# Kernel tuning notes

Hardware: AMD Instinct MI355X
Metric: run time of the kernel (lower is better)

Reference implementation:

```python
import jax, jax.numpy as jnp
import numpy as np


def setup_inputs() -> dict:
    key = jax.random.key(0)
    ks = jax.random.split(key, 7)
    SEQ, B, IN, H, OUT = 1024, 1024, 57, 128, 18
    return {
        "line_tensor": jax.random.normal(ks[0], (SEQ, B, IN), dtype=jnp.float32),
        "W_ih": jax.random.normal(ks[1], (H, IN), dtype=jnp.float32) * 0.1,
        "b_ih": jax.random.normal(ks[2], (H,), dtype=jnp.float32) * 0.1,
        "W_hh": jax.random.normal(ks[3], (H, H), dtype=jnp.float32) * 0.1,
        "b_hh": jax.random.normal(ks[4], (H,), dtype=jnp.float32) * 0.1,
        "W_ho": jax.random.normal(ks[5], (OUT, H), dtype=jnp.float32) * 0.1,
        "b_ho": jax.random.normal(ks[6], (OUT,), dtype=jnp.float32) * 0.1,
    }


def reference(line_tensor, W_ih, b_ih, W_hh, b_hh, W_ho, b_ho):
    # Elman RNN: h_t = tanh(i2h(x_t) + h2h(h_{t-1})); output = log_softmax(h2o(h_T))
    B = line_tensor.shape[1]
    H = W_hh.shape[0]
    h0 = jnp.zeros((B, H), dtype=line_tensor.dtype)

    def step(h, x):  # x: [B, IN], h: [B, H]
        h = jnp.tanh(x @ W_ih.T + b_ih + h @ W_hh.T + b_hh)
        return h, None

    hT, _ = jax.lax.scan(step, h0, line_tensor)
    logits = hT @ W_ho.T + b_ho  # [B, OUT]
    out = jax.nn.log_softmax(logits, axis=1)
    return (out, hT)
```

## Files before the change

### kernel.cpp

```cpp
#include <hip/hip_runtime.h>
#include <math.h>

#define SEQ   1024
#define BATCH 1024
#define IN_F  57
#define H_F   128
#define OUT_F 18
#define MROWS 16
#define HSTR  136
#define XSTR  72
#define NT    512

typedef __attribute__((ext_vector_type(8))) short bf8;
typedef __attribute__((ext_vector_type(4))) float f32x4;

static __device__ __forceinline__ short f2bf(float f) {
    unsigned u = __builtin_bit_cast(unsigned, f);
    u = (u + 0x7FFFu + ((u >> 16) & 1u)) >> 16;
    return (short)u;
}
static __device__ __forceinline__ float bf2f(short s) {
    unsigned u = ((unsigned)(unsigned short)s) << 16;
    return __builtin_bit_cast(float, u);
}

__global__ __launch_bounds__(NT) void rnn_mfma_kernel(
    const float* __restrict__ X,
    const float* __restrict__ W_ih,
    const float* __restrict__ b_ih,
    const float* __restrict__ W_hh,
    const float* __restrict__ b_hh,
    const float* __restrict__ W_ho,
    const float* __restrict__ b_ho,
    float* __restrict__ out)
{
    const int tid  = threadIdx.x;
    const int lane = tid & 63;
    const int wv   = tid >> 6;
    const int n16  = lane & 15;
    const int quad = lane >> 4;
    const int b0   = blockIdx.x * MROWS;

    __shared__ short h_lds[2][MROWS][HSTR];
    __shared__ short x_lds[2][MROWS][XSTR];
    __shared__ float logits_lds[MROWS][OUT_F];
    __shared__ float red_lds[MROWS][2];

    const int j0 = wv * 16 + n16;

    const float* wp0 = W_hh + j0 * H_F + quad * 8;
#define LDW8(P) ({ \
        f32x4 p_ = *(const f32x4*)(P); \
        f32x4 q_ = *(const f32x4*)((P) + 4); \
        bf8 f_; \
        f_[0]=f2bf(p_[0]); f_[1]=f2bf(p_[1]); f_[2]=f2bf(p_[2]); f_[3]=f2bf(p_[3]); \
        f_[4]=f2bf(q_[0]); f_[5]=f2bf(q_[1]); f_[6]=f2bf(q_[2]); f_[7]=f2bf(q_[3]); \
        f_; })
    bf8 wh0 = LDW8(wp0 +  0), wh1 = LDW8(wp0 + 32), wh2 = LDW8(wp0 + 64), wh3 = LDW8(wp0 + 96);

#define LDWI(J, KS) ({ \
        bf8 f_; \
        _Pragma("unroll") \
        for (int i_ = 0; i_ < 8; ++i_) { \
            int k_ = (KS) * 32 + quad * 8 + i_; \
            f_[i_] = (k_ < IN_F) ? f2bf(W_ih[(J) * IN_F + k_]) : (short)0; \
        } f_; })
    bf8 wi0 = LDWI(j0, 0), wi1 = LDWI(j0, 1);

    const float bias0 = b_ih[j0] + b_hh[j0];

    const bool  xlane = (tid < 228);
    const size_t tstride = (size_t)BATCH * IN_F;
    const float* xbase = X + (size_t)b0 * IN_F + tid * 4;
    int xm[4], xk[4];
    #pragma unroll
    for (int e = 0; e < 4; ++e) {
        int idx = tid * 4 + e;
        xm[e] = (int)((unsigned)idx / 57u);
        xk[e] = idx - xm[e] * 57;
    }

    for (int i = tid; i < MROWS * HSTR; i += NT) (&h_lds[0][0][0])[i] = 0;
    for (int i = tid; i < 2 * MROWS * XSTR; i += NT) (&x_lds[0][0][0])[i] = 0;
    f32x4 xq0 = {0,0,0,0}, xq1 = {0,0,0,0};
    if (xlane) {
        f32x4 v = *(const f32x4*)(xbase);
        #pragma unroll
        for (int e = 0; e < 4; ++e) x_lds[0][xm[e]][xk[e]] = f2bf(v[e]);
        xq1 = *(const f32x4*)(xbase + 1 * tstride);
        xq0 = *(const f32x4*)(xbase + 2 * tstride);
    }
    __syncthreads();

#define STEP_BARRIER() do { \
        asm volatile("s_waitcnt lgkmcnt(0)" ::: "memory"); \
        __builtin_amdgcn_s_barrier(); \
    } while (0)

#define MFMA __builtin_amdgcn_mfma_f32_16x16x32_bf16
#define STEP(CB, NB, T, XS) do { \
         \
        const short* hc = &h_lds[CB][0][0] + n16 * HSTR + quad * 8; \
        const short* xc = &x_lds[CB][0][0] + n16 * XSTR + quad * 8; \
        bf8 ah0 = *(const bf8*)(hc +  0); \
        bf8 ah1 = *(const bf8*)(hc + 32); \
        bf8 ah2 = *(const bf8*)(hc + 64); \
        bf8 ah3 = *(const bf8*)(hc + 96); \
        bf8 ax0 = *(const bf8*)(xc +  0); \
        bf8 ax1 = *(const bf8*)(xc + 32); \
         \
        if (((T) + 1 < SEQ) && xlane) { \
            _Pragma("unroll") \
            for (int e = 0; e < 4; ++e) x_lds[NB][xm[e]][xk[e]] = f2bf(XS[e]); \
        } \
         \
        if (((T) + 3 < SEQ) && xlane) \
            XS = *(const f32x4*)(xbase + (size_t)((T) + 3) * tstride); \
         \
        f32x4 ca = {bias0, bias0, bias0, bias0}, cb = {0.f, 0.f, 0.f, 0.f}; \
        ca = MFMA(ah0, wh0, ca, 0, 0, 0); \
        cb = MFMA(ah1, wh1, cb, 0, 0, 0); \
        ca = MFMA(ah2, wh2, ca, 0, 0, 0); \
        cb = MFMA(ah3, wh3, cb, 0, 0, 0); \
        ca = MFMA(ax0, wi0, ca, 0, 0, 0); \
        cb = MFMA(ax1, wi1, cb, 0, 0, 0); \
        short* hn = &h_lds[NB][0][0]; \
        _Pragma("unroll") \
        for (int r = 0; r < 4; ++r) { \
            int m = quad * 4 + r; \
            float z = fminf(fmaxf(ca[r] + cb[r], -9.f), 9.f); \
            float e = __expf(2.f * z); \
            hn[m * HSTR + j0] = f2bf((e - 1.f) * __builtin_amdgcn_rcpf(e + 1.f)); \
        } \
        STEP_BARRIER(); \
    } while (0)

    for (int t = 0; t < SEQ; t += 2) {
        STEP(0, 1, t,     xq1);
        STEP(1, 0, t + 1, xq0);
    }
#undef STEP
#undef MFMA

    float* hT = out + (size_t)BATCH * OUT_F;
    #pragma unroll
    for (int r = 0; r < (MROWS * H_F) / NT; ++r) {
        int idx = tid + r * NT;
        int m = idx >> 7, k = idx & 127;
        hT[(size_t)(b0 + m) * H_F + k] = bf2f(h_lds[0][m][k]);
    }

    for (int idx = tid; idx < MROWS * OUT_F; idx += NT) {
        int m = idx / OUT_F, o = idx - m * OUT_F;
        float acc = b_ho[o];
        for (int k = 0; k < H_F; ++k)
            acc = fmaf(bf2f(h_lds[0][m][k]), W_ho[o * H_F + k], acc);
        logits_lds[m][o] = acc;
    }
    __syncthreads();

    if (tid < MROWS) {
        float mx = -1e30f;
        #pragma unroll
        for (int o = 0; o < OUT_F; ++o) mx = fmaxf(mx, logits_lds[tid][o]);
        float s = 0.f;
        #pragma unroll
        for (int o = 0; o < OUT_F; ++o) s += expf(logits_lds[tid][o] - mx);
        red_lds[tid][0] = mx;
        red_lds[tid][1] = logf(s);
    }
    __syncthreads();

    for (int idx = tid; idx < MROWS * OUT_F; idx += NT) {
        int m = idx / OUT_F, o = idx - m * OUT_F;
        out[(size_t)(b0 + m) * OUT_F + o] =
            logits_lds[m][o] - red_lds[m][0] - red_lds[m][1];
    }
}

extern "C" void kernel_launch(void* const* d_in, const int* in_sizes, int n_in,
                              void* d_out, int out_size, void* d_ws, size_t ws_size,
                              hipStream_t stream) {
    const float* X    = (const float*)d_in[0];
    const float* W_ih = (const float*)d_in[1];
    const float* b_ih = (const float*)d_in[2];
    const float* W_hh = (const float*)d_in[3];
    const float* b_hh = (const float*)d_in[4];
    const float* W_ho = (const float*)d_in[5];
    const float* b_ho = (const float*)d_in[6];
    float* out = (float*)d_out;

    rnn_mfma_kernel<<<dim3(BATCH / MROWS), dim3(NT), 0, stream>>>(
        X, W_ih, b_ih, W_hh, b_hh, W_ho, b_ho, out);
}
```

Before: 809.2 us.

## Warp-specialize RNN step: split input projection from recurrent matmul

The 8 waves are split into two roles. Four waves do only the recurrent h@W_hh MFMAs and the tanh, each covering 32 hidden columns. The other four waves compute the input projection plus bias for the next timestep one step ahead, writing fp32 results into a new LDS buffer, and also handle the global x prefetch. This removes the input-projection MFMAs and the x staging from the serial recurrence path. In exchange it adds LDS traffic for the projected inputs and doubles the per-wave MFMA and tanh work on the recurrent waves.

```diff
diff --git a/kernel.cpp b/kernel.cpp
--- a/kernel.cpp
+++ b/kernel.cpp
@@ -9,6 +9,7 @@
 #define MROWS 16
 #define HSTR  136
 #define XSTR  72
+#define XPSTR 28
 #define NT    512
 
 typedef __attribute__((ext_vector_type(8))) short bf8;
@@ -40,55 +41,71 @@
     const int n16  = lane & 15;
     const int quad = lane >> 4;
     const int b0   = blockIdx.x * MROWS;
+    const bool hw  = (wv < 4);
+    const int  wv2 = wv & 3;
 
     __shared__ short h_lds[2][MROWS][HSTR];
     __shared__ short x_lds[2][MROWS][XSTR];
+    __shared__ float xp_lds[2][H_F][XPSTR];
     __shared__ float logits_lds[MROWS][OUT_F];
     __shared__ float red_lds[MROWS][2];
 
-    const int j0 = wv * 16 + n16;
-
-    const float* wp0 = W_hh + j0 * H_F + quad * 8;
+    const int jt0 = wv2 * 32 + n16;
+    const int jt1 = jt0 + 16;
+
+    bf8 f0 = {0,0,0,0,0,0,0,0}, f1 = f0, f2 = f0, f3 = f0;
+    bf8 g0 = f0, g1 = f0, g2 = f0, g3 = f0;
+    float biasx0 = 0.f, biasx1 = 0.f;
+
 #define LDW8(P) ({ \
         f32x4 p_ = *(const f32x4*)(P); \
         f32x4 q_ = *(const f32x4*)((P) + 4); \
-        bf8 f_; \
-        f_[0]=f2bf(p_[0]); f_[1]=f2bf(p_[1]); f_[2]=f2bf(p_[2]); f_[3]=f2bf(p_[3]); \
-        f_[4]=f2bf(q_[0]); f_[5]=f2bf(q_[1]); f_[6]=f2bf(q_[2]); f_[7]=f2bf(q_[3]); \
-        f_; })
-    bf8 wh0 = LDW8(wp0 +  0), wh1 = LDW8(wp0 + 32), wh2 = LDW8(wp0 + 64), wh3 = LDW8(wp0 + 96);
-
+        bf8 r_; \
+        r_[0]=f2bf(p_[0]); r_[1]=f2bf(p_[1]); r_[2]=f2bf(p_[2]); r_[3]=f2bf(p_[3]); \
+        r_[4]=f2bf(q_[0]); r_[5]=f2bf(q_[1]); r_[6]=f2bf(q_[2]); r_[7]=f2bf(q_[3]); \
+        r_; })
 #define LDWI(J, KS) ({ \
-        bf8 f_; \
+        bf8 r_; \
         _Pragma("unroll") \
         for (int i_ = 0; i_ < 8; ++i_) { \
             int k_ = (KS) * 32 + quad * 8 + i_; \
-            f_[i_] = (k_ < IN_F) ? f2bf(W_ih[(J) * IN_F + k_]) : (short)0; \
-        } f_; })
-    bf8 wi0 = LDWI(j0, 0), wi1 = LDWI(j0, 1);
-
-    const float bias0 = b_ih[j0] + b_hh[j0];
-
-    const bool  xlane = (tid < 228);
+            r_[i_] = (k_ < IN_F) ? f2bf(W_ih[(J) * IN_F + k_]) : (short)0; \
+        } r_; })
+
+    if (hw) {
+        const float* wp0 = W_hh + jt0 * H_F + quad * 8;
+        const float* wp1 = W_hh + jt1 * H_F + quad * 8;
+        f0 = LDW8(wp0 +  0); f1 = LDW8(wp0 + 32); f2 = LDW8(wp0 + 64); f3 = LDW8(wp0 + 96);
+        g0 = LDW8(wp1 +  0); g1 = LDW8(wp1 + 32); g2 = LDW8(wp1 + 64); g3 = LDW8(wp1 + 96);
+    } else {
+        f0 = LDWI(jt0, 0); f1 = LDWI(jt0, 1);
+        g0 = LDWI(jt1, 0); g1 = LDWI(jt1, 1);
+        biasx0 = b_ih[jt0] + b_hh[jt0];
+        biasx1 = b_ih[jt1] + b_hh[jt1];
+    }
+
+    const int  tid2  = hw ? 0 : (tid - 256);
+    const bool xlane = (!hw) && (tid2 < 228);
     const size_t tstride = (size_t)BATCH * IN_F;
-    const float* xbase = X + (size_t)b0 * IN_F + tid * 4;
+    const float* xbase = X + (size_t)b0 * IN_F + tid2 * 4;
     int xm[4], xk[4];
     #pragma unroll
     for (int e = 0; e < 4; ++e) {
-        int idx = tid * 4 + e;
+        int idx = tid2 * 4 + e;
         xm[e] = (int)((unsigned)idx / 57u);
         xk[e] = idx - xm[e] * 57;
     }
 
     for (int i = tid; i < MROWS * HSTR; i += NT) (&h_lds[0][0][0])[i] = 0;
     for (int i = tid; i < 2 * MROWS * XSTR; i += NT) (&x_lds[0][0][0])[i] = 0;
-    f32x4 xq0 = {0,0,0,0}, xq1 = {0,0,0,0};
+    f32x4 xr1 = {0,0,0,0}, xqA = {0,0,0,0}, xqB = {0,0,0,0};
     if (xlane) {
-        f32x4 v = *(const f32x4*)(xbase);
+        f32x4 v = *(const f32x4*)xbase;
         #pragma unroll
         for (int e = 0; e < 4; ++e) x_lds[0][xm[e]][xk[e]] = f2bf(v[e]);
-        xq1 = *(const f32x4*)(xbase + 1 * tstride);
-        xq0 = *(const f32x4*)(xbase + 2 * tstride);
+        xr1 = *(const f32x4*)(xbase + 1 * tstride);
+        xqA = *(const f32x4*)(xbase + 2 * tstride);
+        xqB = *(const f32x4*)(xbase + 3 * tstride);
     }
     __syncthreads();
 
@@ -98,48 +115,81 @@
     } while (0)
 
 #define MFMA __builtin_amdgcn_mfma_f32_16x16x32_bf16
-#define STEP(CB, NB, T, XS) do { \
-         \
-        const short* hc = &h_lds[CB][0][0] + n16 * HSTR + quad * 8; \
-        const short* xc = &x_lds[CB][0][0] + n16 * XSTR + quad * 8; \
+
+#define XPCOMPUTE(SRC, DST) do { \
+        const short* xc_ = &x_lds[SRC][0][0] + n16 * XSTR + quad * 8; \
+        bf8 ax0_ = *(const bf8*)(xc_ +  0); \
+        bf8 ax1_ = *(const bf8*)(xc_ + 32); \
+        f32x4 c0_ = {biasx0, biasx0, biasx0, biasx0}; \
+        f32x4 c1_ = {biasx1, biasx1, biasx1, biasx1}; \
+        c0_ = MFMA(ax0_, f0, c0_, 0, 0, 0); \
+        c1_ = MFMA(ax0_, g0, c1_, 0, 0, 0); \
+        c0_ = MFMA(ax1_, f1, c0_, 0, 0, 0); \
+        c1_ = MFMA(ax1_, g1, c1_, 0, 0, 0); \
+        *(f32x4*)&xp_lds[DST][jt0][quad * 4] = c0_; \
+        *(f32x4*)&xp_lds[DST][jt1][quad * 4] = c1_; \
+    } while (0)
+
+    if (!hw) {
+        XPCOMPUTE(0, 0);
+        if (xlane) {
+            #pragma unroll
+            for (int e = 0; e < 4; ++e) x_lds[1][xm[e]][xk[e]] = f2bf(xr1[e]);
+        }
+    }
+    STEP_BARRIER();
+
+#define HSTEP(P) do { \
+        const short* hc = &h_lds[P][0][0] + n16 * HSTR + quad * 8; \
+        f32x4 ca = *(const f32x4*)&xp_lds[P][jt0][quad * 4]; \
+        f32x4 cb = *(const f32x4*)&xp_lds[P][jt1][quad * 4]; \
         bf8 ah0 = *(const bf8*)(hc +  0); \
         bf8 ah1 = *(const bf8*)(hc + 32); \
         bf8 ah2 = *(const bf8*)(hc + 64); \
         bf8 ah3 = *(const bf8*)(hc + 96); \
-        bf8 ax0 = *(const bf8*)(xc +  0); \
-        bf8 ax1 = *(const bf8*)(xc + 32); \
-         \
-        if (((T) + 1 < SEQ) && xlane) { \
-            _Pragma("unroll") \
-            for (int e = 0; e < 4; ++e) x_lds[NB][xm[e]][xk[e]] = f2bf(XS[e]); \
-        } \
-         \
-        if (((T) + 3 < SEQ) && xlane) \
-            XS = *(const f32x4*)(xbase + (size_t)((T) + 3) * tstride); \
-         \
-        f32x4 ca = {bias0, bias0, bias0, bias0}, cb = {0.f, 0.f, 0.f, 0.f}; \
-        ca = MFMA(ah0, wh0, ca, 0, 0, 0); \
-        cb = MFMA(ah1, wh1, cb, 0, 0, 0); \
-        ca = MFMA(ah2, wh2, ca, 0, 0, 0); \
-        cb = MFMA(ah3, wh3, cb, 0, 0, 0); \
-        ca = MFMA(ax0, wi0, ca, 0, 0, 0); \
-        cb = MFMA(ax1, wi1, cb, 0, 0, 0); \
-        short* hn = &h_lds[NB][0][0]; \
+        f32x4 da = {0.f,0.f,0.f,0.f}, db = {0.f,0.f,0.f,0.f}; \
+        ca = MFMA(ah0, f0, ca, 0, 0, 0); \
+        cb = MFMA(ah0, g0, cb, 0, 0, 0); \
+        da = MFMA(ah2, f2, da, 0, 0, 0); \
+        db = MFMA(ah2, g2, db, 0, 0, 0); \
+        ca = MFMA(ah1, f1, ca, 0, 0, 0); \
+        cb = MFMA(ah1, g1, cb, 0, 0, 0); \
+        da = MFMA(ah3, f3, da, 0, 0, 0); \
+        db = MFMA(ah3, g3, db, 0, 0, 0); \
+        short* hn = &h_lds[P ^ 1][0][0]; \
         _Pragma("unroll") \
         for (int r = 0; r < 4; ++r) { \
             int m = quad * 4 + r; \
-            float z = fminf(fmaxf(ca[r] + cb[r], -9.f), 9.f); \
-            float e = __expf(2.f * z); \
-            hn[m * HSTR + j0] = f2bf((e - 1.f) * __builtin_amdgcn_rcpf(e + 1.f)); \
+            float z0 = fminf(fmaxf(ca[r] + da[r], -9.f), 9.f); \
+            float e0 = __expf(2.f * z0); \
+            hn[m * HSTR + jt0] = f2bf((e0 - 1.f) * __builtin_amdgcn_rcpf(e0 + 1.f)); \
+            float z1 = fminf(fmaxf(cb[r] + db[r], -9.f), 9.f); \
+            float e1 = __expf(2.f * z1); \
+            hn[m * HSTR + jt1] = f2bf((e1 - 1.f) * __builtin_amdgcn_rcpf(e1 + 1.f)); \
         } \
-        STEP_BARRIER(); \
+    } while (0)
+
+#define XSTEP(P, T, XS) do { \
+        if ((T) + 1 < SEQ) { \
+            XPCOMPUTE(P ^ 1, P ^ 1); \
+            if (((T) + 2 < SEQ) && xlane) { \
+                _Pragma("unroll") \
+                for (int e = 0; e < 4; ++e) x_lds[P][xm[e]][xk[e]] = f2bf(XS[e]); \
+            } \
+            if (((T) + 4 < SEQ) && xlane) \
+                XS = *(const f32x4*)(xbase + (size_t)((T) + 4) * tstride); \
+        } \
     } while (0)
 
     for (int t = 0; t < SEQ; t += 2) {
-        STEP(0, 1, t,     xq1);
-        STEP(1, 0, t + 1, xq0);
-    }
-#undef STEP
+        if (hw) HSTEP(0); else XSTEP(0, t, xqA);
+        STEP_BARRIER();
+        if (hw) HSTEP(1); else XSTEP(1, t + 1, xqB);
+        STEP_BARRIER();
+    }
+#undef HSTEP
+#undef XSTEP
+#undef XPCOMPUTE
 #undef MFMA
 
     float* hT = out + (size_t)BATCH * OUT_F;
```

New measurement: 806.8 us. About the same (-0.3%).
